# Kernel optimization log

Measured on AMD Instinct MI355X. Metric: run time of the kernel, lower is better.

## Reference

```python
import jax, jax.numpy as jnp
import numpy as np


def setup_inputs() -> dict:
    key = jax.random.key(0)
    k1, k2, k3 = jax.random.split(key, 3)
    S, B, H, D = 1024, 32, 512, 1024  # max_len, batch, bin_rnn_size, bin_rep_size
    hidden = jax.random.normal(k1, (2, B, H), dtype=jnp.float32)
    encoder_outputs = jax.random.normal(k2, (S, B, D), dtype=jnp.float32)
    # nn.Linear(D, D) params; scale W for numerically sane softmax logits
    W = jax.random.normal(k3, (D, D), dtype=jnp.float32) / np.float32(np.sqrt(D))
    b = jnp.zeros((D,), dtype=jnp.float32)
    return {"hidden": hidden, "encoder_outputs": encoder_outputs, "W": W, "b": b}


def reference(hidden, encoder_outputs, W, b):
    # method == 'general'
    B = hidden.shape[1]
    # torch.reshape((-1, B, 2H)).squeeze() == C-order flatten -> [B, 2H]
    h = hidden.reshape(B, -1)                                   # [B, D]
    energy = jnp.einsum('sbd,ed->sbe', encoder_outputs, W) + b  # Linear: x @ W.T + b
    # batch_product_luong + sum over features == contraction
    attn_energies = jnp.einsum('bd,sbd->bs', h, energy)         # [B, S]
    alpha = jax.nn.softmax(attn_energies, axis=1)[:, None, :]   # [B, 1, S]
    # alpha.bmm(encoder_outputs.transpose(0,1)) -> [B, 1, D]
    reps = jnp.einsum('bos,sbd->bod', alpha, encoder_outputs)
    return (reps, alpha)
```

## Files before the change

### kernel.cpp

```cpp
#include <hip/hip_runtime.h>
#include <stdint.h>

#define S 1024
#define B 32
#define D 1024
#define NCH 32
#define CH (S / NCH)
#define NPAIR (CH / 2)
#define ECH 8
#define EC 128

#define PG_OFF   0
#define LOG_OFF  (PG_OFF + ECH * B * D)
#define MARR_OFF (LOG_OFF + B * S)
#define LARR_OFF (MARR_OFF + NCH * B)
#define PACC_OFF (LARR_OFF + NCH * B)

typedef const __attribute__((address_space(1))) unsigned int* gas_t;
typedef __attribute__((address_space(3))) unsigned int* las_t;

__global__ __launch_bounds__(256) void kG(const float* __restrict__ hid,
                                          const float* __restrict__ W,
                                          float* __restrict__ ws) {
    const int d  = blockIdx.x * 256 + threadIdx.x;
    const int b  = blockIdx.y;
    const int e0 = blockIdx.z * EC;
    const float* __restrict__ hrow = hid + b * D;
    float acc = 0.f;
    #pragma unroll 8
    for (int e = e0; e < e0 + EC; ++e)
        acc = fmaf(hrow[e], W[(size_t)e * D + d], acc);
    ws[PG_OFF + ((size_t)blockIdx.z * B + b) * D + d] = acc;
}

__global__ __launch_bounds__(256) void kB(const float* __restrict__ enc,
                                          float* __restrict__ ws) {
    const int tid  = threadIdx.x;
    const int lane = tid & 63;
    const int wid  = tid >> 6;
    const int c    = blockIdx.x;
    const int b    = blockIdx.y;

    float* pg     = ws + PG_OFF;
    float* logits = ws + LOG_OFF;
    float* marr   = ws + MARR_OFF;
    float* larr   = ws + LARR_OFF;
    float* pacc   = ws + PACC_OFF;

    __shared__ float tile[2][2 * D];
    __shared__ float red[2][2][4];

    const int row0 = c * CH;

    auto stage = [&](int buf, int p) {
        #pragma unroll
        for (int r = 0; r < 2; ++r) {
            const float* gp = enc + ((size_t)(row0 + 2 * p + r) * B + b) * D
                            + wid * 256 + lane * 4;
            float* lp = &tile[buf][r * D + wid * 256];
            __builtin_amdgcn_global_load_lds((gas_t)(uintptr_t)gp,
                                             (las_t)(uintptr_t)lp, 16, 0, 0);
        }
    };

    stage(0, 0);

    float4 gv = {0.f, 0.f, 0.f, 0.f};
    #pragma unroll
    for (int ec = 0; ec < ECH; ++ec) {
        float4 v = ((const float4*)(pg + (size_t)(ec * B + b) * D))[tid];
        gv.x += v.x; gv.y += v.y; gv.z += v.z; gv.w += v.w;
    }
    __syncthreads();

    float m = -3.0e38f, l = 0.f;
    float4 acc = {0.f, 0.f, 0.f, 0.f};

    for (int p = 0; p < NPAIR; ++p) {
        const int cur = p & 1;
        if (p + 1 < NPAIR) stage(cur ^ 1, p + 1);

        const float4* t4 = (const float4*)tile[cur];
        float4 e0 = t4[tid];
        float4 e1 = t4[256 + tid];
        float pd0 = e0.x * gv.x + e0.y * gv.y + e0.z * gv.z + e0.w * gv.w;
        float pd1 = e1.x * gv.x + e1.y * gv.y + e1.z * gv.z + e1.w * gv.w;
        #pragma unroll
        for (int off = 1; off < 64; off <<= 1) {
            pd0 += __shfl_xor(pd0, off, 64);
            pd1 += __shfl_xor(pd1, off, 64);
        }
        if (lane == 0) { red[p & 1][0][wid] = pd0; red[p & 1][1][wid] = pd1; }
        __syncthreads();

        float l0 = red[p & 1][0][0] + red[p & 1][0][1]
                 + red[p & 1][0][2] + red[p & 1][0][3];
        float l1 = red[p & 1][1][0] + red[p & 1][1][1]
                 + red[p & 1][1][2] + red[p & 1][1][3];
        if (tid == 0) {
            logits[b * S + row0 + 2 * p]     = l0;
            logits[b * S + row0 + 2 * p + 1] = l1;
        }
        float mn  = fmaxf(m, l0);
        float sc0 = __expf(m - mn);
        float pA  = __expf(l0 - mn);
        float mn2 = fmaxf(mn, l1);
        float sc1 = __expf(mn - mn2);
        float pB  = __expf(l1 - mn2);
        float s01 = sc0 * sc1;
        float a0  = pA * sc1;
        l = l * s01 + a0 + pB;
        acc.x = acc.x * s01 + a0 * e0.x + pB * e1.x;
        acc.y = acc.y * s01 + a0 * e0.y + pB * e1.y;
        acc.z = acc.z * s01 + a0 * e0.z + pB * e1.z;
        acc.w = acc.w * s01 + a0 * e0.w + pB * e1.w;
        m = mn2;
    }

    ((float4*)pacc)[(size_t)(c * B + b) * (D / 4) + tid] = acc;
    if (tid == 0) { marr[c * B + b] = m; larr[c * B + b] = l; }
}

__global__ __launch_bounds__(256) void kC(float* __restrict__ out,
                                          const float* __restrict__ ws) {
    const int tid = threadIdx.x;
    const int q   = blockIdx.x;
    const int b   = blockIdx.y;
    const float* logits = ws + LOG_OFF;
    const float* marr   = ws + MARR_OFF;
    const float* larr   = ws + LARR_OFF;
    const float* pacc   = ws + PACC_OFF;

    __shared__ float shm[NCH], shl[NCH], shf[NCH];
    if (tid < NCH) { shm[tid] = marr[tid * B + b]; shl[tid] = larr[tid * B + b]; }
    __syncthreads();
    float mg = -3.0e38f;
    #pragma unroll
    for (int cc = 0; cc < NCH; ++cc) mg = fmaxf(mg, shm[cc]);
    if (tid < NCH) shf[tid] = __expf(shm[tid] - mg);
    __syncthreads();
    float lg = 0.f;
    #pragma unroll
    for (int cc = 0; cc < NCH; ++cc) lg += shl[cc] * shf[cc];
    const float inv = 1.f / lg;

    if (tid < 64) {
        const int d4 = q * 64 + tid;
        float4 racc = {0.f, 0.f, 0.f, 0.f};
        #pragma unroll 4
        for (int cc = 0; cc < NCH; ++cc) {
            float  fc = shf[cc];
            float4 v  = ((const float4*)pacc)[(size_t)(cc * B + b) * (D / 4) + d4];
            racc.x += v.x * fc; racc.y += v.y * fc;
            racc.z += v.z * fc; racc.w += v.w * fc;
        }
        float4 rep = {racc.x * inv, racc.y * inv, racc.z * inv, racc.w * inv};
        ((float4*)out)[b * (D / 4) + d4] = rep;
    }
    const int s = q * 256 + tid;
    out[B * D + b * S + s] = __expf(logits[b * S + s] - mg) * inv;
}

extern "C" void kernel_launch(void* const* d_in, const int* in_sizes, int n_in,
                              void* d_out, int out_size, void* d_ws, size_t ws_size,
                              hipStream_t stream) {
    const float* hid = (const float*)d_in[0];
    const float* enc = (const float*)d_in[1];
    const float* W   = (const float*)d_in[2];

    float* out = (float*)d_out;
    float* ws  = (float*)d_ws;

    kG<<<dim3(D / 256, B, ECH), 256, 0, stream>>>(hid, W, ws);
    kB<<<dim3(NCH, B), 256, 0, stream>>>(enc, ws);
    kC<<<dim3(4, B), 256, 0, stream>>>(out, ws);
}
```

Before: 43.85 us.

## Restructure hidden-times-W GEMV to read W once and add reduction kernel

The projection of the hidden state through W is reorganised so each block stages a slice of the hidden vectors for all batches in shared memory. Each element of W is then loaded once and reused across every batch row, instead of being re-read once per batch. The partial sums over 32 e-chunks are combined by a new small kernel, kR, which writes a single reduced vector, so kB now does one load instead of summing partials. In exchange there is an extra kernel launch, a larger partial buffer, and a reduction kernel with only 32 blocks.

New measurement: 42.12 us. 1.04x faster.

```diff
diff --git a/kernel.cpp b/kernel.cpp
--- a/kernel.cpp
+++ b/kernel.cpp
@@ -7,11 +7,12 @@
 #define NCH 32
 #define CH (S / NCH)
 #define NPAIR (CH / 2)
-#define ECH 8
-#define EC 128
+#define GECH 32
+#define GEC 32
 
 #define PG_OFF   0
-#define LOG_OFF  (PG_OFF + ECH * B * D)
+#define G_OFF    (PG_OFF + GECH * B * D)
+#define LOG_OFF  (G_OFF + B * D)
 #define MARR_OFF (LOG_OFF + B * S)
 #define LARR_OFF (MARR_OFF + NCH * B)
 #define PACC_OFF (LARR_OFF + NCH * B)
@@ -19,18 +20,48 @@
 typedef const __attribute__((address_space(1))) unsigned int* gas_t;
 typedef __attribute__((address_space(3))) unsigned int* las_t;
 
-__global__ __launch_bounds__(256) void kG(const float* __restrict__ hid,
-                                          const float* __restrict__ W,
-                                          float* __restrict__ ws) {
-    const int d  = blockIdx.x * 256 + threadIdx.x;
-    const int b  = blockIdx.y;
-    const int e0 = blockIdx.z * EC;
-    const float* __restrict__ hrow = hid + b * D;
-    float acc = 0.f;
+__global__ __launch_bounds__(256) void kG3(const float* __restrict__ hid,
+                                           const float* __restrict__ W,
+                                           float* __restrict__ ws) {
+    const int tid = threadIdx.x;
+    const int dc  = blockIdx.x;
+    const int ec  = blockIdx.y;
+    __shared__ float h_sh[GEC * 33];
+    #pragma unroll
+    for (int k = 0; k < (GEC * B) / 256; ++k) {
+        int lin = tid + k * 256;
+        int e = lin & (GEC - 1);
+        int b = lin >> 5;
+        h_sh[e * 33 + b] = hid[b * D + ec * GEC + e];
+    }
+    __syncthreads();
+
+    const int b  = tid >> 3;
+    const int dq = tid & 7;
+    const float4* W4 = (const float4*)W;
+    float4 a4 = {0.f, 0.f, 0.f, 0.f};
     #pragma unroll 8
-    for (int e = e0; e < e0 + EC; ++e)
-        acc = fmaf(hrow[e], W[(size_t)e * D + d], acc);
-    ws[PG_OFF + ((size_t)blockIdx.z * B + b) * D + d] = acc;
+    for (int e = 0; e < GEC; ++e) {
+        float  h = h_sh[e * 33 + b];
+        float4 w = W4[(size_t)(ec * GEC + e) * (D / 4) + dc * 8 + dq];
+        a4.x = fmaf(h, w.x, a4.x);
+        a4.y = fmaf(h, w.y, a4.y);
+        a4.z = fmaf(h, w.z, a4.z);
+        a4.w = fmaf(h, w.w, a4.w);
+    }
+    ((float4*)(ws + PG_OFF + ((size_t)ec * B + b) * D + dc * 32))[dq] = a4;
+}
+
+__global__ __launch_bounds__(256) void kR(float* __restrict__ ws) {
+    const int idx = blockIdx.x * 256 + threadIdx.x;
+    const float4* pg4 = (const float4*)(ws + PG_OFF);
+    float4 s4 = {0.f, 0.f, 0.f, 0.f};
+    #pragma unroll
+    for (int ec = 0; ec < GECH; ++ec) {
+        float4 v = pg4[(size_t)ec * (B * D / 4) + idx];
+        s4.x += v.x; s4.y += v.y; s4.z += v.z; s4.w += v.w;
+    }
+    ((float4*)(ws + G_OFF))[idx] = s4;
 }
 
 __global__ __launch_bounds__(256) void kB(const float* __restrict__ enc,
@@ -41,7 +72,7 @@
     const int c    = blockIdx.x;
     const int b    = blockIdx.y;
 
-    float* pg     = ws + PG_OFF;
+    const float* g = ws + G_OFF;
     float* logits = ws + LOG_OFF;
     float* marr   = ws + MARR_OFF;
     float* larr   = ws + LARR_OFF;
@@ -65,12 +96,7 @@
 
     stage(0, 0);
 
-    float4 gv = {0.f, 0.f, 0.f, 0.f};
-    #pragma unroll
-    for (int ec = 0; ec < ECH; ++ec) {
-        float4 v = ((const float4*)(pg + (size_t)(ec * B + b) * D))[tid];
-        gv.x += v.x; gv.y += v.y; gv.z += v.z; gv.w += v.w;
-    }
+    float4 gv = ((const float4*)(g + b * D))[tid];
     __syncthreads();
 
     float m = -3.0e38f, l = 0.f;
@@ -171,7 +197,8 @@
     float* out = (float*)d_out;
     float* ws  = (float*)d_ws;
 
-    kG<<<dim3(D / 256, B, ECH), 256, 0, stream>>>(hid, W, ws);
+    kG3<<<dim3(32, GECH), 256, 0, stream>>>(hid, W, ws);
+    kR<<<dim3(32), 256, 0, stream>>>(ws);
     kB<<<dim3(NCH, B), 256, 0, stream>>>(enc, ws);
     kC<<<dim3(4, B), 256, 0, stream>>>(out, ws);
 }
```
